# Optimization experiments

Hardware: AMD Instinct MI355X
Metric: run time of the kernel (lower is better)

The kernel has to match this reference:

```python
import jax, jax.numpy as jnp
import numpy as np

D_MODEL = 1024
NUM_HEADS = 16
D_K = D_MODEL // NUM_HEADS


def setup_inputs() -> dict:
    key = jax.random.key(0)
    ks = jax.random.split(key, 5)
    s = 1.0 / np.sqrt(D_MODEL)  # xavier-ish scale
    x = jax.random.normal(ks[0], (2, 2048, D_MODEL), dtype=jnp.float32)
    Wq = jax.random.normal(ks[1], (D_MODEL, D_MODEL), dtype=jnp.float32) * s
    Wk = jax.random.normal(ks[2], (D_MODEL, D_MODEL), dtype=jnp.float32) * s
    Wv = jax.random.normal(ks[3], (D_MODEL, D_MODEL), dtype=jnp.float32) * s
    Wo = jax.random.normal(ks[4], (D_MODEL, D_MODEL), dtype=jnp.float32) * s
    z = jnp.zeros((D_MODEL,), dtype=jnp.float32)
    return {"x": x, "Wq": Wq, "bq": z, "Wk": Wk, "bk": z, "Wv": Wv, "bv": z, "Wo": Wo, "bo": z}


def reference(x, Wq, bq, Wk, bk, Wv, bv, Wo, bo):
    B, S, _ = x.shape
    # torch Linear: y = x @ W.T + b
    def split_heads(t):
        return t.reshape(B, S, NUM_HEADS, D_K).transpose(0, 2, 1, 3)  # [B,H,S,Dk]
    q = split_heads(x @ Wq.T + bq)
    k = split_heads(x @ Wk.T + bk)
    v = split_heads(x @ Wv.T + bv)
    scores = jnp.einsum('bhqd,bhkd->bhqk', q, k) / jnp.sqrt(jnp.float32(D_K))
    attn = jax.nn.softmax(scores, axis=-1)
    out = jnp.einsum('bhqk,bhkd->bhqd', attn, v)  # [B,H,S,Dk]
    out = out.transpose(0, 2, 1, 3).reshape(B, S, D_MODEL)
    return out @ Wo.T + bo
```

## Files before the change

kernel.cpp:

```cpp
#include <hip/hip_runtime.h>
#include <hip/hip_bf16.h>
#include <type_traits>


typedef __attribute__((ext_vector_type(4))) float f32x4;
typedef __attribute__((ext_vector_type(16))) float f32x16;
typedef __attribute__((ext_vector_type(8))) short s16x8;
typedef __attribute__((ext_vector_type(4))) unsigned int u32x4;

#define GLDS16(g, l)                                                       \
  __builtin_amdgcn_global_load_lds(                                        \
      (const __attribute__((address_space(1))) unsigned int*)(g),          \
      (__attribute__((address_space(3))) unsigned int*)(l), 16, 0, 0)

#define SCALE_Q 0.18033688011112042f

__device__ __forceinline__ unsigned short f2bf(float f) {
  unsigned int u = __builtin_bit_cast(unsigned int, f);
  u += 0x7fffu + ((u >> 16) & 1u);
  return (unsigned short)(u >> 16);
}

__device__ __forceinline__ unsigned int cvtpk_bf16(float lo, float hi) {
  unsigned int r;
  asm("v_cvt_pk_bf16_f32 %0, %1, %2" : "=v"(r) : "v"(lo), "v"(hi));
  return r;
}

__device__ __forceinline__ float fexp2(float x) {
  return __builtin_amdgcn_exp2f(x);
}

__global__ void cvt_all(const float* __restrict__ x, const float* __restrict__ Wq,
                        const float* __restrict__ Wk, const float* __restrict__ Wv,
                        const float* __restrict__ Wo, const float* __restrict__ bq,
                        const float* __restrict__ bk, const float* __restrict__ bv,
                        unsigned short* __restrict__ xb,
                        unsigned short* __restrict__ wcat,
                        unsigned short* __restrict__ wob,
                        float* __restrict__ bcat) {
  int g = blockIdx.x * blockDim.x + threadIdx.x;
  if (g >= 2097152) {
    int off = (g - 2097152) * 4;
    const float* src;
    float sc = 1.0f;
    int o2 = off;
    if (off < 1024) {
      src = bq; sc = SCALE_Q;
    } else if (off < 2048) {
      src = bk; o2 = off - 1024;
    } else {
      src = bv; o2 = off - 2048;
    }
    float4 v = *reinterpret_cast<const float4*>(src + o2);
    float4 w;
    w.x = v.x * sc; w.y = v.y * sc; w.z = v.z * sc; w.w = v.w * sc;
    *reinterpret_cast<float4*>(bcat + off) = w;
    return;
  }
  const float* in;
  unsigned short* out;
  int off;
  float scale = 1.0f;
  if (g < 1048576) {
    in = x; out = xb; off = g;
  } else if (g < 1310720) {
    in = Wq; out = wcat; off = g - 1048576; scale = SCALE_Q;
  } else if (g < 1572864) {
    in = Wk; out = wcat + 1048576; off = g - 1310720;
  } else if (g < 1835008) {
    in = Wv; out = wcat + 2097152; off = g - 1572864;
  } else {
    in = Wo; out = wob; off = g - 1835008;
  }
  float4 v = *reinterpret_cast<const float4*>(in + off * 4);
  ushort4 o;
  o.x = f2bf(v.x * scale); o.y = f2bf(v.y * scale);
  o.z = f2bf(v.z * scale); o.w = f2bf(v.w * scale);
  *reinterpret_cast<ushort4*>(out + off * 4) = o;
}

template <typename CT, bool VSPLIT>
__global__ __launch_bounds__(256, 2) void gemm_bt(
    const unsigned short* __restrict__ A, const unsigned short* __restrict__ B,
    CT* __restrict__ C, unsigned short* __restrict__ vtp, int M, int N, int K,
    const float* __restrict__ bias) {
  __shared__ unsigned short As[128 * 32];
  __shared__ unsigned short Bs[128 * 32];
  const int tid = threadIdx.x;
  const int wv = tid >> 6, lane = tid & 63;
  const int g = lane >> 4, c16 = lane & 15;
  const int wm = wv >> 1, wn = wv & 1;
  const int bm = blockIdx.y, bn = blockIdx.x;

  const unsigned short* Ab = A + (size_t)bm * 128 * K;
  const unsigned short* Bb = B + (size_t)bn * 128 * K;

  f32x4 acc[4][4] = {};

  for (int k0 = 0; k0 < K; k0 += 32) {
    __syncthreads();
#pragma unroll
    for (int r = 0; r < 2; ++r) {
      int i = r * 256 + tid;
      int row = i >> 2, col = (i & 3) * 8;
      GLDS16(Ab + (size_t)row * K + k0 + col, &As[i * 8]);
    }
#pragma unroll
    for (int r = 0; r < 2; ++r) {
      int i = r * 256 + tid;
      int row = i >> 2, col = (i & 3) * 8;
      GLDS16(Bb + (size_t)row * K + k0 + col, &Bs[i * 8]);
    }
    __syncthreads();

    s16x8 af[4], bfv[4];
#pragma unroll
    for (int m = 0; m < 4; ++m)
      af[m] = *(const s16x8*)&As[(wm * 64 + m * 16 + c16) * 32 + g * 8];
#pragma unroll
    for (int n = 0; n < 4; ++n)
      bfv[n] = *(const s16x8*)&Bs[(wn * 64 + n * 16 + c16) * 32 + g * 8];
#pragma unroll
    for (int m = 0; m < 4; ++m)
#pragma unroll
      for (int n = 0; n < 4; ++n)
        acc[m][n] = __builtin_amdgcn_mfma_f32_16x16x32_bf16(af[m], bfv[n],
                                                            acc[m][n], 0, 0, 0);
  }

#pragma unroll
  for (int m = 0; m < 4; ++m) {
#pragma unroll
    for (int n = 0; n < 4; ++n) {
      int col = bn * 128 + wn * 64 + n * 16 + c16;
      float bb = bias ? bias[col] : 0.f;
      if constexpr (VSPLIT) {
        if (col >= 2048) {
          int d = col - 2048, hh = d >> 6, dl = d & 63;
          int row0 = bm * 128 + wm * 64 + m * 16 + g * 4;
          int b_ = row0 >> 11, s = row0 & 2047;
          ushort4 pk;
          pk.x = f2bf(acc[m][n][0] + bb);
          pk.y = f2bf(acc[m][n][1] + bb);
          pk.z = f2bf(acc[m][n][2] + bb);
          pk.w = f2bf(acc[m][n][3] + bb);
          *reinterpret_cast<ushort4*>(
              vtp + ((size_t)((b_ * 16 + hh) * 64 + dl)) * 2048 + s) = pk;
          continue;
        }
      }
#pragma unroll
      for (int j = 0; j < 4; ++j) {
        int row = bm * 128 + wm * 64 + m * 16 + g * 4 + j;
        float v = acc[m][n][j] + bb;
        if constexpr (std::is_same<CT, float>::value)
          C[(size_t)row * N + col] = v;
        else
          C[(size_t)row * N + col] = f2bf(v);
      }
    }
  }
}

__global__ __launch_bounds__(1024) void flash_attn(
    const unsigned short* __restrict__ qkv, const unsigned short* __restrict__ vt,
    unsigned short* __restrict__ attn) {
  __shared__ __align__(16) char smem[131072];
  unsigned short* KsB = (unsigned short*)smem;
  unsigned short* VTsB = (unsigned short*)(smem + 65536);
  float* MoB = (float*)smem;
  float* MlB = (float*)(smem + 66560);

  const int tid = threadIdx.x;
  const int wv = tid >> 6, lane = tid & 63;
  const int half = wv >> 3, w8 = wv & 7;
  const int col = lane & 31, hi = lane >> 5;
  const int bh = blockIdx.x, qt = blockIdx.y;
  const int b = bh >> 4, h = bh & 15;
  const int qrow0 = qt * 256 + w8 * 32;

  const int stid = tid & 511;
  const int srow = stid >> 3, scs = stid & 7;
  const int sqc = ((scs - (srow >> 3)) & 7) ^ (srow & 7);
  const int kbase = half * 1024;
  const unsigned short* kgsrc =
      qkv + (size_t)(b * 2048 + kbase + srow) * 3072 + 1024 + h * 64 + sqc * 8;
  const unsigned short* vgsrc =
      vt + (size_t)(bh * 64 + srow) * 2048 + kbase + sqc * 8;

  s16x8 qb[4];
#pragma unroll
  for (int ds = 0; ds < 4; ++ds)
    qb[ds] = *(const s16x8*)(qkv + (size_t)(b * 2048 + qrow0 + col) * 3072 +
                             h * 64 + ds * 16 + hi * 8);

  s16x8 onev;
#pragma unroll
  for (int j = 0; j < 8; ++j) onev[j] = (short)0x3F80;

  f32x16 o[2] = {};
  f32x16 lacc = {};

  GLDS16(kgsrc, &KsB[(half * 4 + 0) * 4096 + stid * 8]);
  GLDS16(vgsrc, &VTsB[(half * 4 + 0) * 4096 + stid * 8]);
  GLDS16(kgsrc + (size_t)64 * 3072, &KsB[(half * 4 + 1) * 4096 + stid * 8]);
  GLDS16(vgsrc + 64, &VTsB[(half * 4 + 1) * 4096 + stid * 8]);

  for (int kt = 0; kt < 16; ++kt) {
    const int buf = kt & 3;
    const unsigned short* Kc = &KsB[(half * 4 + buf) * 4096];
    const unsigned short* Vc = &VTsB[(half * 4 + buf) * 4096];
    if (kt < 14) {
      const int nb = (kt + 2) & 3;
      GLDS16(kgsrc + (size_t)(kt + 2) * 64 * 3072,
             &KsB[(half * 4 + nb) * 4096 + stid * 8]);
      GLDS16(vgsrc + (kt + 2) * 64, &VTsB[(half * 4 + nb) * 4096 + stid * 8]);
      asm volatile("s_waitcnt vmcnt(4)" ::: "memory");
    } else if (kt == 14) {
      asm volatile("s_waitcnt vmcnt(2)" ::: "memory");
    } else {
      asm volatile("s_waitcnt vmcnt(0)" ::: "memory");
    }
    __builtin_amdgcn_s_barrier();

    f32x16 st[2];
    __builtin_amdgcn_s_setprio(1);
#pragma unroll
    for (int kb = 0; kb < 2; ++kb) {
      f32x16 a = {};
#pragma unroll
      for (int ds = 0; ds < 4; ++ds) {
        int row = kb * 32 + col;
        int cs = ds * 2 + hi;
        int hoff = ((cs ^ (row & 7)) + (row >> 3)) & 7;
        s16x8 ka = *(const s16x8*)&Kc[row * 64 + hoff * 8];
        a = __builtin_amdgcn_mfma_f32_32x32x16_bf16(ka, qb[ds], a, 0, 0, 0);
      }
      st[kb] = a;
    }
    __builtin_amdgcn_s_setprio(0);

#pragma unroll
    for (int kb = 0; kb < 2; ++kb)
#pragma unroll
      for (int r = 0; r < 16; ++r) st[kb][r] = fexp2(st[kb][r]);

#pragma unroll
    for (int kb = 0; kb < 2; ++kb) {
#pragma unroll
      for (int hf = 0; hf < 2; ++hf) {
        const int p0 = hf * 8;
        unsigned int a0 = cvtpk_bf16(st[kb][p0 + 0], st[kb][p0 + 1]);
        unsigned int b0 = cvtpk_bf16(st[kb][p0 + 4], st[kb][p0 + 5]);
        unsigned int a1 = cvtpk_bf16(st[kb][p0 + 2], st[kb][p0 + 3]);
        unsigned int b1 = cvtpk_bf16(st[kb][p0 + 6], st[kb][p0 + 7]);
        asm("v_permlane32_swap_b32 %0, %1" : "+v"(a0), "+v"(b0));
        asm("v_permlane32_swap_b32 %0, %1" : "+v"(a1), "+v"(b1));
        u32x4 pw;
        pw[0] = a0; pw[1] = a1; pw[2] = b0; pw[3] = b1;
        const s16x8 pa = __builtin_bit_cast(s16x8, pw);
        const int ks = kb * 2 + hf;
        __builtin_amdgcn_s_setprio(1);
#pragma unroll
        for (int n = 0; n < 2; ++n) {
          int row = n * 32 + col;
          int cs = ks * 2 + hi;
          int hoff = ((cs ^ (row & 7)) + (row >> 3)) & 7;
          s16x8 vb = *(const s16x8*)&Vc[row * 64 + hoff * 8];
          o[n] = __builtin_amdgcn_mfma_f32_32x32x16_bf16(pa, vb, o[n], 0, 0, 0);
        }
        lacc = __builtin_amdgcn_mfma_f32_32x32x16_bf16(pa, onev, lacc, 0, 0, 0);
        __builtin_amdgcn_s_setprio(0);
      }
    }
  }
  __syncthreads();

  if (half == 1) {
#pragma unroll
    for (int r = 0; r < 16; ++r) {
      int qd = (r & 3) + 8 * (r >> 2) + 4 * hi;
      MoB[(w8 * 32 + qd) * 65 + col] = o[0][r];
      MoB[(w8 * 32 + qd) * 65 + 32 + col] = o[1][r];
      if (col == 0) MlB[w8 * 32 + qd] = lacc[r];
    }
  }
  __syncthreads();
  if (half == 0) {
#pragma unroll
    for (int r = 0; r < 16; ++r) {
      int qd = (r & 3) + 8 * (r >> 2) + 4 * hi;
      float linv = 1.f / (lacc[r] + MlB[w8 * 32 + qd]);
      float v0 = (o[0][r] + MoB[(w8 * 32 + qd) * 65 + col]) * linv;
      float v1 = (o[1][r] + MoB[(w8 * 32 + qd) * 65 + 32 + col]) * linv;
      size_t base = (size_t)(b * 2048 + qrow0 + qd) * 1024 + h * 64;
      attn[base + col] = f2bf(v0);
      attn[base + 32 + col] = f2bf(v1);
    }
  }
}

extern "C" void kernel_launch(void* const* d_in, const int* in_sizes, int n_in,
                              void* d_out, int out_size, void* d_ws, size_t ws_size,
                              hipStream_t stream) {
  const float* x  = (const float*)d_in[0];
  const float* Wq = (const float*)d_in[1];
  const float* bq = (const float*)d_in[2];
  const float* Wk = (const float*)d_in[3];
  const float* bk = (const float*)d_in[4];
  const float* Wv = (const float*)d_in[5];
  const float* bv = (const float*)d_in[6];
  const float* Wo = (const float*)d_in[7];
  const float* bo = (const float*)d_in[8];
  float* out = (float*)d_out;

  char* ws = (char*)d_ws;
  const size_t MB = 1024 * 1024;
  unsigned short* xb   = (unsigned short*)(ws + 0);
  unsigned short* attn = (unsigned short*)(ws + 0);
  unsigned short* wob  = (unsigned short*)(ws + 8 * MB);
  unsigned short* wcat = (unsigned short*)(ws + 10 * MB);
  unsigned short* qkv  = (unsigned short*)(ws + 18 * MB);
  unsigned short* vt   = (unsigned short*)(ws + 42 * MB);
  float* bcat          = (float*)(ws + 50 * MB);

  cvt_all<<<8195, 256, 0, stream>>>(x, Wq, Wk, Wv, Wo, bq, bk, bv, xb, wcat,
                                    wob, bcat);

  gemm_bt<unsigned short, true><<<dim3(24, 32), 256, 0, stream>>>(
      xb, wcat, qkv, vt, 4096, 3072, 1024, bcat);

  flash_attn<<<dim3(32, 8), 1024, 0, stream>>>(qkv, vt, attn);

  gemm_bt<float, false><<<dim3(8, 32), 256, 0, stream>>>(
      attn, wob, out, nullptr, 4096, 1024, 1024, bo);
}
```

Measured before the change: 116.0 us.

## Add dedicated 256x256 QKV GEMM with multi-stage async LDS pipeline

```diff
diff --git a/kernel.cpp b/kernel.cpp
--- a/kernel.cpp
+++ b/kernel.cpp
@@ -80,11 +80,123 @@
   *reinterpret_cast<ushort4*>(out + off * 4) = o;
 }
 
-template <typename CT, bool VSPLIT>
+__device__ __forceinline__ void stg(const unsigned short* __restrict__ src,
+                                    unsigned short* __restrict__ dst, int s_r,
+                                    int s_c, int s_csrc, int kt, int kh) {
+#pragma unroll
+  for (int l = 0; l < 2; ++l) {
+    int rt = l * 128 + s_r;
+    GLDS16(src + (size_t)rt * 1024 + kt * 64 + kh * 32 + s_csrc,
+           dst + kh * 8192 + rt * 32 + s_c);
+  }
+}
+
+__global__ __launch_bounds__(512, 2) void gemm_qkv(
+    const unsigned short* __restrict__ A, const unsigned short* __restrict__ B,
+    unsigned short* __restrict__ C, unsigned short* __restrict__ vtp,
+    const float* __restrict__ bias) {
+  __shared__ __align__(16) unsigned short sm[4 * 256 * 64];
+  unsigned short* As = sm;
+  unsigned short* Bs = sm + 2 * 256 * 64;
+
+  const int tid = threadIdx.x;
+  const int lane = tid & 63, wv = tid >> 6;
+  const int g = lane >> 4, c16 = lane & 15;
+  const int wm = wv >> 2, wn = wv & 3;
+  const int bn = blockIdx.x, bm = blockIdx.y;
+
+  const unsigned short* Ab = A + (size_t)(bm * 256) * 1024;
+  const unsigned short* Bb = B + (size_t)(bn * 256) * 1024;
+
+  const int s_r = tid >> 2;
+  const int s_c = (tid & 3) * 8;
+  const int s_csrc = s_c ^ (((tid >> 5) & 1) << 4);
+  const int rc = (g * 8) ^ ((c16 & 8) << 1);
+
+  f32x4 acc[8][4] = {};
+
+#define PH(slot, nh, ks)                                                     \
+  {                                                                          \
+    __builtin_amdgcn_s_barrier();                                            \
+    s16x8 af[8], bf[2];                                                      \
+    _Pragma("unroll") for (int mf = 0; mf < 8; ++mf)                         \
+        af[mf] = *(const s16x8*)&As[((slot)*2 + (ks)) * 8192 +               \
+                                    (wm * 128 + mf * 16 + c16) * 32 + rc];   \
+    _Pragma("unroll") for (int nf = 0; nf < 2; ++nf)                         \
+        bf[nf] = *(const s16x8*)&Bs[((slot)*2 + (ks)) * 8192 +               \
+                                    (wn * 64 + ((nh)*2 + nf) * 16 + c16) *   \
+                                        32 + rc];                            \
+    __builtin_amdgcn_s_setprio(1);                                           \
+    _Pragma("unroll") for (int mf = 0; mf < 8; ++mf)                         \
+        _Pragma("unroll") for (int nf = 0; nf < 2; ++nf)                     \
+            acc[mf][(nh)*2 + nf] = __builtin_amdgcn_mfma_f32_16x16x32_bf16(  \
+                af[mf], bf[nf], acc[mf][(nh)*2 + nf], 0, 0, 0);              \
+    __builtin_amdgcn_s_setprio(0);                                           \
+  }
+
+  stg(Ab, As + 0 * 16384, s_r, s_c, s_csrc, 0, 0);
+  stg(Bb, Bs + 0 * 16384, s_r, s_c, s_csrc, 0, 0);
+  stg(Ab, As + 0 * 16384, s_r, s_c, s_csrc, 0, 1);
+  stg(Bb, Bs + 0 * 16384, s_r, s_c, s_csrc, 0, 1);
+  stg(Ab, As + 1 * 16384, s_r, s_c, s_csrc, 1, 0);
+
+  for (int i = 0; i < 8; ++i) {
+    const int t1 = 2 * i + 1, t2 = 2 * i + 2, t3 = 2 * i + 3;
+    stg(Bb, Bs + 16384, s_r, s_c, s_csrc, t1, 0);
+    asm volatile("s_waitcnt vmcnt(4)" ::: "memory");
+    PH(0, 0, 0);
+    stg(Ab, As + 16384, s_r, s_c, s_csrc, t1, 1);
+    PH(0, 1, 0);
+    stg(Bb, Bs + 16384, s_r, s_c, s_csrc, t1, 1);
+    PH(0, 0, 1);
+    if (i < 7) stg(Ab, As, s_r, s_c, s_csrc, t2, 0);
+    PH(0, 1, 1);
+    if (i < 7) {
+      stg(Bb, Bs, s_r, s_c, s_csrc, t2, 0);
+      asm volatile("s_waitcnt vmcnt(4)" ::: "memory");
+    } else {
+      asm volatile("s_waitcnt vmcnt(0)" ::: "memory");
+    }
+    PH(1, 0, 0);
+    if (i < 7) stg(Ab, As, s_r, s_c, s_csrc, t2, 1);
+    PH(1, 1, 0);
+    if (i < 7) stg(Bb, Bs, s_r, s_c, s_csrc, t2, 1);
+    PH(1, 0, 1);
+    if (i < 7) stg(Ab, As + 16384, s_r, s_c, s_csrc, t3, 0);
+    PH(1, 1, 1);
+  }
+#undef PH
+
+#pragma unroll
+  for (int mf = 0; mf < 8; ++mf) {
+#pragma unroll
+    for (int nf = 0; nf < 4; ++nf) {
+      int col = bn * 256 + wn * 64 + nf * 16 + c16;
+      float bb = bias[col];
+      int row0 = bm * 256 + wm * 128 + mf * 16 + g * 4;
+      if (col >= 2048) {
+        int d = col - 2048, hh = d >> 6, dl = d & 63;
+        int b_ = row0 >> 11, s = row0 & 2047;
+        ushort4 pk;
+        pk.x = f2bf(acc[mf][nf][0] + bb);
+        pk.y = f2bf(acc[mf][nf][1] + bb);
+        pk.z = f2bf(acc[mf][nf][2] + bb);
+        pk.w = f2bf(acc[mf][nf][3] + bb);
+        *reinterpret_cast<ushort4*>(
+            vtp + ((size_t)((b_ * 16 + hh) * 64 + dl)) * 2048 + s) = pk;
+      } else {
+#pragma unroll
+        for (int j = 0; j < 4; ++j)
+          C[(size_t)(row0 + j) * 3072 + col] = f2bf(acc[mf][nf][j] + bb);
+      }
+    }
+  }
+}
+
+template <typename CT>
 __global__ __launch_bounds__(256, 2) void gemm_bt(
     const unsigned short* __restrict__ A, const unsigned short* __restrict__ B,
-    CT* __restrict__ C, unsigned short* __restrict__ vtp, int M, int N, int K,
-    const float* __restrict__ bias) {
+    CT* __restrict__ C, int M, int N, int K, const float* __restrict__ bias) {
   __shared__ unsigned short As[128 * 32];
   __shared__ unsigned short Bs[128 * 32];
   const int tid = threadIdx.x;
@@ -135,21 +247,6 @@
     for (int n = 0; n < 4; ++n) {
       int col = bn * 128 + wn * 64 + n * 16 + c16;
       float bb = bias ? bias[col] : 0.f;
-      if constexpr (VSPLIT) {
-        if (col >= 2048) {
-          int d = col - 2048, hh = d >> 6, dl = d & 63;
-          int row0 = bm * 128 + wm * 64 + m * 16 + g * 4;
-          int b_ = row0 >> 11, s = row0 & 2047;
-          ushort4 pk;
-          pk.x = f2bf(acc[m][n][0] + bb);
-          pk.y = f2bf(acc[m][n][1] + bb);
-          pk.z = f2bf(acc[m][n][2] + bb);
-          pk.w = f2bf(acc[m][n][3] + bb);
-          *reinterpret_cast<ushort4*>(
-              vtp + ((size_t)((b_ * 16 + hh) * 64 + dl)) * 2048 + s) = pk;
-          continue;
-        }
-      }
 #pragma unroll
       for (int j = 0; j < 4; ++j) {
         int row = bm * 128 + wm * 64 + m * 16 + g * 4 + j;
@@ -328,11 +425,10 @@
   cvt_all<<<8195, 256, 0, stream>>>(x, Wq, Wk, Wv, Wo, bq, bk, bv, xb, wcat,
                                     wob, bcat);
 
-  gemm_bt<unsigned short, true><<<dim3(24, 32), 256, 0, stream>>>(
-      xb, wcat, qkv, vt, 4096, 3072, 1024, bcat);
+  gemm_qkv<<<dim3(12, 16), 512, 0, stream>>>(xb, wcat, qkv, vt, bcat);
 
   flash_attn<<<dim3(32, 8), 1024, 0, stream>>>(qkv, vt, attn);
 
-  gemm_bt<float, false><<<dim3(8, 32), 256, 0, stream>>>(
-      attn, wob, out, nullptr, 4096, 1024, 1024, bo);
-}
+  gemm_bt<float><<<dim3(8, 32), 256, 0, stream>>>(
+      attn, wob, out, 4096, 1024, 1024, bo);
+}
```

Measured after the change: 115.6 us. Within noise of the previous version (-0.3%).

## Triple-buffer GEMM LDS tiles with async prefetch, swizzle, and MFMA priority

Applied to the files above, without the earlier changes.

```diff
diff --git a/kernel.cpp b/kernel.cpp
--- a/kernel.cpp
+++ b/kernel.cpp
@@ -81,70 +81,93 @@
 }
 
 template <typename CT, bool VSPLIT>
-__global__ __launch_bounds__(256, 2) void gemm_bt(
+__global__ __launch_bounds__(256, 3) void gemm128(
     const unsigned short* __restrict__ A, const unsigned short* __restrict__ B,
-    CT* __restrict__ C, unsigned short* __restrict__ vtp, int M, int N, int K,
+    CT* __restrict__ C, unsigned short* __restrict__ vtp, int N,
     const float* __restrict__ bias) {
-  __shared__ unsigned short As[128 * 32];
-  __shared__ unsigned short Bs[128 * 32];
+  __shared__ __align__(16) unsigned short As[3 * 128 * 32];
+  __shared__ __align__(16) unsigned short Bs[3 * 128 * 32];
+
   const int tid = threadIdx.x;
-  const int wv = tid >> 6, lane = tid & 63;
+  const int lane = tid & 63, wv = tid >> 6;
   const int g = lane >> 4, c16 = lane & 15;
   const int wm = wv >> 1, wn = wv & 1;
-  const int bm = blockIdx.y, bn = blockIdx.x;
-
-  const unsigned short* Ab = A + (size_t)bm * 128 * K;
-  const unsigned short* Bb = B + (size_t)bn * 128 * K;
+  const int bn = blockIdx.x, bm = blockIdx.y;
+
+  const unsigned short* Ab = A + (size_t)(bm * 128) * 1024;
+  const unsigned short* Bb = B + (size_t)(bn * 128) * 1024;
+
+  const int r0 = tid >> 2, cc0 = (tid & 3) * 8;
+  const int r1 = r0 + 64, cc1 = cc0;
+  const int cs0 = cc0 ^ ((r0 & 8) << 1);
+  const int cs1 = cc1 ^ ((r1 & 8) << 1);
+  const int rc = (g * 8) ^ ((c16 & 8) << 1);
 
   f32x4 acc[4][4] = {};
 
-  for (int k0 = 0; k0 < K; k0 += 32) {
-    __syncthreads();
-#pragma unroll
-    for (int r = 0; r < 2; ++r) {
-      int i = r * 256 + tid;
-      int row = i >> 2, col = (i & 3) * 8;
-      GLDS16(Ab + (size_t)row * K + k0 + col, &As[i * 8]);
-    }
-#pragma unroll
-    for (int r = 0; r < 2; ++r) {
-      int i = r * 256 + tid;
-      int row = i >> 2, col = (i & 3) * 8;
-      GLDS16(Bb + (size_t)row * K + k0 + col, &Bs[i * 8]);
-    }
-    __syncthreads();
-
-    s16x8 af[4], bfv[4];
-#pragma unroll
-    for (int m = 0; m < 4; ++m)
-      af[m] = *(const s16x8*)&As[(wm * 64 + m * 16 + c16) * 32 + g * 8];
-#pragma unroll
-    for (int n = 0; n < 4; ++n)
-      bfv[n] = *(const s16x8*)&Bs[(wn * 64 + n * 16 + c16) * 32 + g * 8];
-#pragma unroll
-    for (int m = 0; m < 4; ++m)
-#pragma unroll
-      for (int n = 0; n < 4; ++n)
-        acc[m][n] = __builtin_amdgcn_mfma_f32_16x16x32_bf16(af[m], bfv[n],
-                                                            acc[m][n], 0, 0, 0);
-  }
-
-#pragma unroll
-  for (int m = 0; m < 4; ++m) {
-#pragma unroll
-    for (int n = 0; n < 4; ++n) {
-      int col = bn * 128 + wn * 64 + n * 16 + c16;
-      float bb = bias ? bias[col] : 0.f;
+#define STG(mat, base, kt, slot)                                           \
+  {                                                                        \
+    GLDS16(base + (size_t)r0 * 1024 + (kt) * 32 + cs0,                     \
+           mat + (slot) * 4096 + r0 * 32 + cc0);                           \
+    GLDS16(base + (size_t)r1 * 1024 + (kt) * 32 + cs1,                     \
+           mat + (slot) * 4096 + r1 * 32 + cc1);                           \
+  }
+
+  STG(As, Ab, 0, 0)
+  STG(Bs, Bb, 0, 0)
+  STG(As, Ab, 1, 1)
+  STG(Bs, Bb, 1, 1)
+
+  int slot = 0, slot2 = 2;
+  for (int t = 0; t < 32; ++t) {
+    if (t < 31) {
+      asm volatile("s_waitcnt vmcnt(4)" ::: "memory");
+    } else {
+      asm volatile("s_waitcnt vmcnt(0)" ::: "memory");
+    }
+    __builtin_amdgcn_s_barrier();
+    if (t < 30) {
+      STG(As, Ab, t + 2, slot2)
+      STG(Bs, Bb, t + 2, slot2)
+    }
+    s16x8 af[4], bf[4];
+#pragma unroll
+    for (int mf = 0; mf < 4; ++mf)
+      af[mf] = *(const s16x8*)&As[slot * 4096 +
+                                  (wm * 64 + mf * 16 + c16) * 32 + rc];
+#pragma unroll
+    for (int nf = 0; nf < 4; ++nf)
+      bf[nf] = *(const s16x8*)&Bs[slot * 4096 +
+                                  (wn * 64 + nf * 16 + c16) * 32 + rc];
+    __builtin_amdgcn_s_setprio(1);
+#pragma unroll
+    for (int mf = 0; mf < 4; ++mf)
+#pragma unroll
+      for (int nf = 0; nf < 4; ++nf)
+        acc[mf][nf] = __builtin_amdgcn_mfma_f32_16x16x32_bf16(
+            af[mf], bf[nf], acc[mf][nf], 0, 0, 0);
+    __builtin_amdgcn_s_setprio(0);
+    slot = (slot == 2) ? 0 : slot + 1;
+    slot2 = (slot2 == 2) ? 0 : slot2 + 1;
+  }
+#undef STG
+
+#pragma unroll
+  for (int mf = 0; mf < 4; ++mf) {
+#pragma unroll
+    for (int nf = 0; nf < 4; ++nf) {
+      int col = bn * 128 + wn * 64 + nf * 16 + c16;
+      float bb = bias[col];
+      int row0 = bm * 128 + wm * 64 + mf * 16 + g * 4;
       if constexpr (VSPLIT) {
         if (col >= 2048) {
           int d = col - 2048, hh = d >> 6, dl = d & 63;
-          int row0 = bm * 128 + wm * 64 + m * 16 + g * 4;
           int b_ = row0 >> 11, s = row0 & 2047;
           ushort4 pk;
-          pk.x = f2bf(acc[m][n][0] + bb);
-          pk.y = f2bf(acc[m][n][1] + bb);
-          pk.z = f2bf(acc[m][n][2] + bb);
-          pk.w = f2bf(acc[m][n][3] + bb);
+          pk.x = f2bf(acc[mf][nf][0] + bb);
+          pk.y = f2bf(acc[mf][nf][1] + bb);
+          pk.z = f2bf(acc[mf][nf][2] + bb);
+          pk.w = f2bf(acc[mf][nf][3] + bb);
           *reinterpret_cast<ushort4*>(
               vtp + ((size_t)((b_ * 16 + hh) * 64 + dl)) * 2048 + s) = pk;
           continue;
@@ -152,12 +175,11 @@
       }
 #pragma unroll
       for (int j = 0; j < 4; ++j) {
-        int row = bm * 128 + wm * 64 + m * 16 + g * 4 + j;
-        float v = acc[m][n][j] + bb;
+        float v = acc[mf][nf][j] + bb;
         if constexpr (std::is_same<CT, float>::value)
-          C[(size_t)row * N + col] = v;
+          C[(size_t)(row0 + j) * N + col] = v;
         else
-          C[(size_t)row * N + col] = f2bf(v);
+          C[(size_t)(row0 + j) * N + col] = f2bf(v);
       }
     }
   }
@@ -328,11 +350,11 @@
   cvt_all<<<8195, 256, 0, stream>>>(x, Wq, Wk, Wv, Wo, bq, bk, bv, xb, wcat,
                                     wob, bcat);
 
-  gemm_bt<unsigned short, true><<<dim3(24, 32), 256, 0, stream>>>(
-      xb, wcat, qkv, vt, 4096, 3072, 1024, bcat);
+  gemm128<unsigned short, true><<<dim3(24, 32), 256, 0, stream>>>(
+      xb, wcat, qkv, vt, 3072, bcat);
 
   flash_attn<<<dim3(32, 8), 1024, 0, stream>>>(qkv, vt, attn);
 
-  gemm_bt<float, false><<<dim3(8, 32), 256, 0, stream>>>(
-      attn, wob, out, nullptr, 4096, 1024, 1024, bo);
-}
+  gemm128<float, false><<<dim3(8, 32), 256, 0, stream>>>(
+      attn, wob, out, nullptr, 1024, bo);
+}
```

Result: faster. 112.7 us (-2.8%).
